# Kernel optimization log

Measured on AMD Instinct MI355X. Metric: run time of the kernel, lower is better.

Reference implementation:

```python
import jax, jax.numpy as jnp
import numpy as np


def _skew(v):
    # v: [B,3] -> [B,3,3] skew-symmetric matrices
    z = jnp.zeros_like(v[:, 0])
    return jnp.stack([
        jnp.stack([z, -v[:, 2], v[:, 1]], axis=-1),
        jnp.stack([v[:, 2], z, -v[:, 0]], axis=-1),
        jnp.stack([-v[:, 1], v[:, 0], z], axis=-1),
    ], axis=-2)


def _so3_exp(phi):
    # phi: [B,3] -> [B,3,3] rotation matrices via Rodrigues formula
    theta_sq = jnp.sum(phi * phi, axis=-1)            # [B]
    small = theta_sq < 1e-8
    theta_sq_safe = jnp.where(small, 1.0, theta_sq)
    theta = jnp.sqrt(theta_sq_safe)
    A = jnp.where(small, 1.0 - theta_sq / 6.0, jnp.sin(theta) / theta)
    Bc = jnp.where(small, 0.5 - theta_sq / 24.0, (1.0 - jnp.cos(theta)) / theta_sq_safe)
    K = _skew(phi)                                    # [B,3,3]
    I = jnp.eye(3, dtype=phi.dtype)
    return I + A[:, None, None] * K + Bc[:, None, None] * (K @ K)


def setup_inputs() -> dict:
    key = jax.random.key(0)
    k1, = jax.random.split(key, 1)
    B, T = 4096, 1024
    imu = jax.random.normal(k1, (B, 6, T), dtype=jnp.float32) * 0.5  # gyro + accel
    t = jnp.broadcast_to(jnp.arange(T, dtype=jnp.float32) * 0.005, (B, T))  # 200 Hz
    x = jnp.concatenate([t[:, None, :], imu], axis=1)  # [B,7,T]
    return {"x": x}


def reference(x) -> jnp.ndarray:
    # x: [B,7,T] -> y: [B,15] = [DC (9), DV (3), DR (3)] per window
    Bn = x.shape[0]
    t = x[:, 0, :]                          # [B,T]
    dt = (t[:, 1:] - t[:, :-1]).T           # [T-1,B]
    w = jnp.moveaxis(x[:, 1:4, :-1], 2, 0)  # [T-1,B,3] gyro at idx-1
    a = jnp.moveaxis(x[:, 4:7, :-1], 2, 0)  # [T-1,B,3] accel at idx-1

    DC0 = jnp.broadcast_to(jnp.eye(3, dtype=x.dtype), (Bn, 3, 3))
    DV0 = jnp.zeros((Bn, 3), dtype=x.dtype)
    DR0 = jnp.zeros((Bn, 3), dtype=x.dtype)

    def step(carry, inp):
        DC, DV, DR = carry
        dt_k, w_k, a_k = inp                         # [B], [B,3], [B,3]
        dtc = dt_k[:, None]
        DCa = jnp.einsum('bij,bj->bi', DC, a_k)      # [B,3]
        DR = DR + DV * dtc + 0.5 * DCa * dtc * dtc
        DV = DV + DCa * dtc
        DC = DC @ _so3_exp(w_k * dtc)
        return (DC, DV, DR), None

    (DC, DV, DR), _ = jax.lax.scan(step, (DC0, DV0, DR0), (dt, w, a))
    return jnp.concatenate([DC.reshape(Bn, 9), DV, DR], axis=-1)  # [B,15]
```

## Files before the change

kernel.cpp:

```cpp
#include <hip/hip_runtime.h>

#define T_LEN 1024
#define NSTEP 1023
#define SPT   16

struct El {
    float c0,c1,c2,c3,c4,c5,c6,c7,c8;
    float v0,v1,v2;
    float r0,r1,r2;
    float tau;
};

__device__ __forceinline__ El compose(const El& a, const El& b) {
    El o;
    o.r0 = a.r0 + a.v0*b.tau + a.c0*b.r0 + a.c1*b.r1 + a.c2*b.r2;
    o.r1 = a.r1 + a.v1*b.tau + a.c3*b.r0 + a.c4*b.r1 + a.c5*b.r2;
    o.r2 = a.r2 + a.v2*b.tau + a.c6*b.r0 + a.c7*b.r1 + a.c8*b.r2;
    o.v0 = a.v0 + a.c0*b.v0 + a.c1*b.v1 + a.c2*b.v2;
    o.v1 = a.v1 + a.c3*b.v0 + a.c4*b.v1 + a.c5*b.v2;
    o.v2 = a.v2 + a.c6*b.v0 + a.c7*b.v1 + a.c8*b.v2;
    o.c0 = a.c0*b.c0 + a.c1*b.c3 + a.c2*b.c6;
    o.c1 = a.c0*b.c1 + a.c1*b.c4 + a.c2*b.c7;
    o.c2 = a.c0*b.c2 + a.c1*b.c5 + a.c2*b.c8;
    o.c3 = a.c3*b.c0 + a.c4*b.c3 + a.c5*b.c6;
    o.c4 = a.c3*b.c1 + a.c4*b.c4 + a.c5*b.c7;
    o.c5 = a.c3*b.c2 + a.c4*b.c5 + a.c5*b.c8;
    o.c6 = a.c6*b.c0 + a.c7*b.c3 + a.c8*b.c6;
    o.c7 = a.c6*b.c1 + a.c7*b.c4 + a.c8*b.c7;
    o.c8 = a.c6*b.c2 + a.c7*b.c5 + a.c8*b.c8;
    o.tau = a.tau + b.tau;
    return o;
}

__device__ __forceinline__ El shfl_down_el(const El& e, int delta) {
    El o;
    o.c0 = __shfl_down(e.c0, delta);
    o.c1 = __shfl_down(e.c1, delta);
    o.c2 = __shfl_down(e.c2, delta);
    o.c3 = __shfl_down(e.c3, delta);
    o.c4 = __shfl_down(e.c4, delta);
    o.c5 = __shfl_down(e.c5, delta);
    o.c6 = __shfl_down(e.c6, delta);
    o.c7 = __shfl_down(e.c7, delta);
    o.c8 = __shfl_down(e.c8, delta);
    o.v0 = __shfl_down(e.v0, delta);
    o.v1 = __shfl_down(e.v1, delta);
    o.v2 = __shfl_down(e.v2, delta);
    o.r0 = __shfl_down(e.r0, delta);
    o.r1 = __shfl_down(e.r1, delta);
    o.r2 = __shfl_down(e.r2, delta);
    o.tau = __shfl_down(e.tau, delta);
    return o;
}

__device__ __forceinline__ void so3_exp(float px, float py, float pz, float R[9]) {
    float t2 = px*px + py*py + pz*pz;
    float A, Bc;
    if (t2 < 1e-2f) {
        float t4 = t2*t2;
        A  = 1.0f - t2*(1.0f/6.0f)  + t4*(1.0f/120.0f);
        Bc = 0.5f - t2*(1.0f/24.0f) + t4*(1.0f/720.0f);
    } else {
        float th = sqrtf(t2);
        A = __sinf(th)/th;
        float sh = __sinf(0.5f*th);
        Bc = 2.0f*sh*sh/t2;
    }
    float xx = px*px, yy = py*py, zz = pz*pz;
    float xy = px*py, xz = px*pz, yz = py*pz;
    R[0] = 1.0f - Bc*(yy+zz);
    R[1] = Bc*xy - A*pz;
    R[2] = Bc*xz + A*py;
    R[3] = Bc*xy + A*pz;
    R[4] = 1.0f - Bc*(xx+zz);
    R[5] = Bc*yz - A*px;
    R[6] = Bc*xz - A*py;
    R[7] = Bc*yz + A*px;
    R[8] = 1.0f - Bc*(xx+yy);
}

extern "C" __global__ void __launch_bounds__(256)
rmi_kernel(const float* __restrict__ x, float* __restrict__ out, int B) {
    const int lane = threadIdx.x & 63;
    const int wid  = threadIdx.x >> 6;
    const int b    = blockIdx.x * 4 + wid;
    if (b >= B) return;
    const float* __restrict__ xb = x + (size_t)b * (7 * T_LEN);
    const int k0 = lane * SPT;

    El e = {1.f,0.f,0.f, 0.f,1.f,0.f, 0.f,0.f,1.f,
            0.f,0.f,0.f, 0.f,0.f,0.f, 0.f};

#pragma unroll
    for (int c = 0; c < SPT/4; ++c) {
        const int kc = k0 + 4*c;
        float4 t4  = *reinterpret_cast<const float4*>(xb + kc);
        float  tn  = (kc + 4 < T_LEN) ? xb[kc + 4] : 0.0f;
        float4 wx4 = *reinterpret_cast<const float4*>(xb + 1*T_LEN + kc);
        float4 wy4 = *reinterpret_cast<const float4*>(xb + 2*T_LEN + kc);
        float4 wz4 = *reinterpret_cast<const float4*>(xb + 3*T_LEN + kc);
        float4 ax4 = *reinterpret_cast<const float4*>(xb + 4*T_LEN + kc);
        float4 ay4 = *reinterpret_cast<const float4*>(xb + 5*T_LEN + kc);
        float4 az4 = *reinterpret_cast<const float4*>(xb + 6*T_LEN + kc);

        float tv[5]  = {t4.x, t4.y, t4.z, t4.w, tn};
        float wxv[4] = {wx4.x, wx4.y, wx4.z, wx4.w};
        float wyv[4] = {wy4.x, wy4.y, wy4.z, wy4.w};
        float wzv[4] = {wz4.x, wz4.y, wz4.z, wz4.w};
        float axv[4] = {ax4.x, ax4.y, ax4.z, ax4.w};
        float ayv[4] = {ay4.x, ay4.y, ay4.z, ay4.w};
        float azv[4] = {az4.x, az4.y, az4.z, az4.w};

#pragma unroll
        for (int j = 0; j < 4; ++j) {
            const int k = kc + j;
            if (k < NSTEP) {
                float dt = tv[j+1] - tv[j];
                float ax = axv[j], ay = ayv[j], az = azv[j];
                float Ca0 = e.c0*ax + e.c1*ay + e.c2*az;
                float Ca1 = e.c3*ax + e.c4*ay + e.c5*az;
                float Ca2 = e.c6*ax + e.c7*ay + e.c8*az;
                float h = 0.5f * dt * dt;
                e.r0 += e.v0*dt + Ca0*h;
                e.r1 += e.v1*dt + Ca1*h;
                e.r2 += e.v2*dt + Ca2*h;
                e.v0 += Ca0*dt;
                e.v1 += Ca1*dt;
                e.v2 += Ca2*dt;
                float Rk[9];
                so3_exp(wxv[j]*dt, wyv[j]*dt, wzv[j]*dt, Rk);
                float n0 = e.c0*Rk[0] + e.c1*Rk[3] + e.c2*Rk[6];
                float n1 = e.c0*Rk[1] + e.c1*Rk[4] + e.c2*Rk[7];
                float n2 = e.c0*Rk[2] + e.c1*Rk[5] + e.c2*Rk[8];
                float n3 = e.c3*Rk[0] + e.c4*Rk[3] + e.c5*Rk[6];
                float n4 = e.c3*Rk[1] + e.c4*Rk[4] + e.c5*Rk[7];
                float n5 = e.c3*Rk[2] + e.c4*Rk[5] + e.c5*Rk[8];
                float n6 = e.c6*Rk[0] + e.c7*Rk[3] + e.c8*Rk[6];
                float n7 = e.c6*Rk[1] + e.c7*Rk[4] + e.c8*Rk[7];
                float n8 = e.c6*Rk[2] + e.c7*Rk[5] + e.c8*Rk[8];
                e.c0=n0; e.c1=n1; e.c2=n2;
                e.c3=n3; e.c4=n4; e.c5=n5;
                e.c6=n6; e.c7=n7; e.c8=n8;
                e.tau += dt;
            }
        }
    }

#pragma unroll
    for (int str = 1; str < 64; str <<= 1) {
        El o = shfl_down_el(e, str);
        e = compose(e, o);
    }

    if (lane == 0) {
        float* ob = out + (size_t)b * 15;
        ob[0]=e.c0;  ob[1]=e.c1;  ob[2]=e.c2;
        ob[3]=e.c3;  ob[4]=e.c4;  ob[5]=e.c5;
        ob[6]=e.c6;  ob[7]=e.c7;  ob[8]=e.c8;
        ob[9]=e.v0;  ob[10]=e.v1; ob[11]=e.v2;
        ob[12]=e.r0; ob[13]=e.r1; ob[14]=e.r2;
    }
}

extern "C" void kernel_launch(void* const* d_in, const int* in_sizes, int n_in,
                              void* d_out, int out_size, void* d_ws, size_t ws_size,
                              hipStream_t stream) {
    const float* x = (const float*)d_in[0];
    float* out = (float*)d_out;
    const int B = in_sizes[0] / (7 * T_LEN);
    rmi_kernel<<<(B + 3) / 4, 256, 0, stream>>>(x, out, B);
}
```

Baseline: 179.6 us.

## Split each window across a full block with cross-wave LDS composition

Each batch window is now handled by a 256-thread block instead of a single wave, so every thread integrates 4 steps instead of 16. The per-wave shuffle scan results are written to shared memory and composed serially by thread 0 to produce the output. This shortens the serial per-thread chain and raises parallelism, in exchange for 4x more blocks, a block barrier, and more shuffle-reduction work per window overall. The B bounds check is dropped because the grid now has exactly B blocks.

After: 165.8 us. 7.7% less time.

```diff
diff --git a/kernel.cpp b/kernel.cpp
--- a/kernel.cpp
+++ b/kernel.cpp
@@ -2,7 +2,6 @@
 
 #define T_LEN 1024
 #define NSTEP 1023
-#define SPT   16
 
 struct El {
     float c0,c1,c2,c3,c4,c5,c6,c7,c8;
@@ -80,69 +79,67 @@
 }
 
 extern "C" __global__ void __launch_bounds__(256)
-rmi_kernel(const float* __restrict__ x, float* __restrict__ out, int B) {
-    const int lane = threadIdx.x & 63;
-    const int wid  = threadIdx.x >> 6;
-    const int b    = blockIdx.x * 4 + wid;
-    if (b >= B) return;
+rmi_kernel(const float* __restrict__ x, float* __restrict__ out) {
+    const int tid  = threadIdx.x;
+    const int lane = tid & 63;
+    const int wid  = tid >> 6;
+    const int b    = blockIdx.x;
     const float* __restrict__ xb = x + (size_t)b * (7 * T_LEN);
-    const int k0 = lane * SPT;
+
+    __shared__ float s[4 * 17];
+
+    const int k0 = tid * 4;
+    float4 t4  = *reinterpret_cast<const float4*>(xb + k0);
+    float  tn  = (k0 + 4 < T_LEN) ? xb[k0 + 4] : 0.0f;
+    float4 wx4 = *reinterpret_cast<const float4*>(xb + 1*T_LEN + k0);
+    float4 wy4 = *reinterpret_cast<const float4*>(xb + 2*T_LEN + k0);
+    float4 wz4 = *reinterpret_cast<const float4*>(xb + 3*T_LEN + k0);
+    float4 ax4 = *reinterpret_cast<const float4*>(xb + 4*T_LEN + k0);
+    float4 ay4 = *reinterpret_cast<const float4*>(xb + 5*T_LEN + k0);
+    float4 az4 = *reinterpret_cast<const float4*>(xb + 6*T_LEN + k0);
+
+    float tv[5]  = {t4.x, t4.y, t4.z, t4.w, tn};
+    float wxv[4] = {wx4.x, wx4.y, wx4.z, wx4.w};
+    float wyv[4] = {wy4.x, wy4.y, wy4.z, wy4.w};
+    float wzv[4] = {wz4.x, wz4.y, wz4.z, wz4.w};
+    float axv[4] = {ax4.x, ax4.y, ax4.z, ax4.w};
+    float ayv[4] = {ay4.x, ay4.y, ay4.z, ay4.w};
+    float azv[4] = {az4.x, az4.y, az4.z, az4.w};
 
     El e = {1.f,0.f,0.f, 0.f,1.f,0.f, 0.f,0.f,1.f,
             0.f,0.f,0.f, 0.f,0.f,0.f, 0.f};
 
 #pragma unroll
-    for (int c = 0; c < SPT/4; ++c) {
-        const int kc = k0 + 4*c;
-        float4 t4  = *reinterpret_cast<const float4*>(xb + kc);
-        float  tn  = (kc + 4 < T_LEN) ? xb[kc + 4] : 0.0f;
-        float4 wx4 = *reinterpret_cast<const float4*>(xb + 1*T_LEN + kc);
-        float4 wy4 = *reinterpret_cast<const float4*>(xb + 2*T_LEN + kc);
-        float4 wz4 = *reinterpret_cast<const float4*>(xb + 3*T_LEN + kc);
-        float4 ax4 = *reinterpret_cast<const float4*>(xb + 4*T_LEN + kc);
-        float4 ay4 = *reinterpret_cast<const float4*>(xb + 5*T_LEN + kc);
-        float4 az4 = *reinterpret_cast<const float4*>(xb + 6*T_LEN + kc);
-
-        float tv[5]  = {t4.x, t4.y, t4.z, t4.w, tn};
-        float wxv[4] = {wx4.x, wx4.y, wx4.z, wx4.w};
-        float wyv[4] = {wy4.x, wy4.y, wy4.z, wy4.w};
-        float wzv[4] = {wz4.x, wz4.y, wz4.z, wz4.w};
-        float axv[4] = {ax4.x, ax4.y, ax4.z, ax4.w};
-        float ayv[4] = {ay4.x, ay4.y, ay4.z, ay4.w};
-        float azv[4] = {az4.x, az4.y, az4.z, az4.w};
-
-#pragma unroll
-        for (int j = 0; j < 4; ++j) {
-            const int k = kc + j;
-            if (k < NSTEP) {
-                float dt = tv[j+1] - tv[j];
-                float ax = axv[j], ay = ayv[j], az = azv[j];
-                float Ca0 = e.c0*ax + e.c1*ay + e.c2*az;
-                float Ca1 = e.c3*ax + e.c4*ay + e.c5*az;
-                float Ca2 = e.c6*ax + e.c7*ay + e.c8*az;
-                float h = 0.5f * dt * dt;
-                e.r0 += e.v0*dt + Ca0*h;
-                e.r1 += e.v1*dt + Ca1*h;
-                e.r2 += e.v2*dt + Ca2*h;
-                e.v0 += Ca0*dt;
-                e.v1 += Ca1*dt;
-                e.v2 += Ca2*dt;
-                float Rk[9];
-                so3_exp(wxv[j]*dt, wyv[j]*dt, wzv[j]*dt, Rk);
-                float n0 = e.c0*Rk[0] + e.c1*Rk[3] + e.c2*Rk[6];
-                float n1 = e.c0*Rk[1] + e.c1*Rk[4] + e.c2*Rk[7];
-                float n2 = e.c0*Rk[2] + e.c1*Rk[5] + e.c2*Rk[8];
-                float n3 = e.c3*Rk[0] + e.c4*Rk[3] + e.c5*Rk[6];
-                float n4 = e.c3*Rk[1] + e.c4*Rk[4] + e.c5*Rk[7];
-                float n5 = e.c3*Rk[2] + e.c4*Rk[5] + e.c5*Rk[8];
-                float n6 = e.c6*Rk[0] + e.c7*Rk[3] + e.c8*Rk[6];
-                float n7 = e.c6*Rk[1] + e.c7*Rk[4] + e.c8*Rk[7];
-                float n8 = e.c6*Rk[2] + e.c7*Rk[5] + e.c8*Rk[8];
-                e.c0=n0; e.c1=n1; e.c2=n2;
-                e.c3=n3; e.c4=n4; e.c5=n5;
-                e.c6=n6; e.c7=n7; e.c8=n8;
-                e.tau += dt;
-            }
+    for (int j = 0; j < 4; ++j) {
+        const int k = k0 + j;
+        if (k < NSTEP) {
+            float dt = tv[j+1] - tv[j];
+            float ax = axv[j], ay = ayv[j], az = azv[j];
+            float Ca0 = e.c0*ax + e.c1*ay + e.c2*az;
+            float Ca1 = e.c3*ax + e.c4*ay + e.c5*az;
+            float Ca2 = e.c6*ax + e.c7*ay + e.c8*az;
+            float h = 0.5f * dt * dt;
+            e.r0 += e.v0*dt + Ca0*h;
+            e.r1 += e.v1*dt + Ca1*h;
+            e.r2 += e.v2*dt + Ca2*h;
+            e.v0 += Ca0*dt;
+            e.v1 += Ca1*dt;
+            e.v2 += Ca2*dt;
+            float Rk[9];
+            so3_exp(wxv[j]*dt, wyv[j]*dt, wzv[j]*dt, Rk);
+            float n0 = e.c0*Rk[0] + e.c1*Rk[3] + e.c2*Rk[6];
+            float n1 = e.c0*Rk[1] + e.c1*Rk[4] + e.c2*Rk[7];
+            float n2 = e.c0*Rk[2] + e.c1*Rk[5] + e.c2*Rk[8];
+            float n3 = e.c3*Rk[0] + e.c4*Rk[3] + e.c5*Rk[6];
+            float n4 = e.c3*Rk[1] + e.c4*Rk[4] + e.c5*Rk[7];
+            float n5 = e.c3*Rk[2] + e.c4*Rk[5] + e.c5*Rk[8];
+            float n6 = e.c6*Rk[0] + e.c7*Rk[3] + e.c8*Rk[6];
+            float n7 = e.c6*Rk[1] + e.c7*Rk[4] + e.c8*Rk[7];
+            float n8 = e.c6*Rk[2] + e.c7*Rk[5] + e.c8*Rk[8];
+            e.c0=n0; e.c1=n1; e.c2=n2;
+            e.c3=n3; e.c4=n4; e.c5=n5;
+            e.c6=n6; e.c7=n7; e.c8=n8;
+            e.tau += dt;
         }
     }
 
@@ -153,6 +150,23 @@
     }
 
     if (lane == 0) {
+        float* me = s + wid * 17;
+        me[0]=e.c0;  me[1]=e.c1;  me[2]=e.c2;
+        me[3]=e.c3;  me[4]=e.c4;  me[5]=e.c5;
+        me[6]=e.c6;  me[7]=e.c7;  me[8]=e.c8;
+        me[9]=e.v0;  me[10]=e.v1; me[11]=e.v2;
+        me[12]=e.r0; me[13]=e.r1; me[14]=e.r2;
+        me[15]=e.tau;
+    }
+    __syncthreads();
+    if (tid == 0) {
+#pragma unroll
+        for (int w = 1; w < 4; ++w) {
+            const float* o = s + w * 17;
+            El q = {o[0],o[1],o[2],o[3],o[4],o[5],o[6],o[7],o[8],
+                    o[9],o[10],o[11],o[12],o[13],o[14],o[15]};
+            e = compose(e, q);
+        }
         float* ob = out + (size_t)b * 15;
         ob[0]=e.c0;  ob[1]=e.c1;  ob[2]=e.c2;
         ob[3]=e.c3;  ob[4]=e.c4;  ob[5]=e.c5;
@@ -168,5 +182,5 @@
     const float* x = (const float*)d_in[0];
     float* out = (float*)d_out;
     const int B = in_sizes[0] / (7 * T_LEN);
-    rmi_kernel<<<(B + 3) / 4, 256, 0, stream>>>(x, out, B);
+    rmi_kernel<<<B, 256, 0, stream>>>(x, out);
 }
```
